# Optimization experiments

Measured on AMD Instinct MI355X. Metric: run time of the kernel, lower is better.

Reference implementation:

```python
import jax, jax.numpy as jnp
import numpy as np

B, C, W, T = 4, 64, 128, 20


def _sinusoid_table(t, c):
    # angle[ch, tau] = tau / 10000^(2*(ch//2)/C); even ch -> sin, odd ch -> cos
    pos = jnp.arange(t, dtype=jnp.float32)                       # [t]
    ch = jnp.arange(c)                                           # [C]
    inv_freq = jnp.power(10000.0, -2.0 * (ch // 2).astype(jnp.float32) / c)  # [C]
    angle = inv_freq[:, None] * pos[None, :]                     # [C, t]
    pe = jnp.where((ch % 2 == 0)[:, None], jnp.sin(angle), jnp.cos(angle))   # [C, t]
    return pe


def setup_inputs() -> dict:
    key = jax.random.key(0)
    x = jax.random.normal(key, (B, C, W, W, T), dtype=jnp.float32)
    return {"x": x, "t": T}


def reference(x, t):
    # x: [B, C, W, W, t]; pos_table broadcast over batch and spatial dims
    pe = _sinusoid_table(t, x.shape[1])          # [C, t]
    return x + pe[None, :, None, None, :]
```

## Files before the change

### kernel.cpp

```cpp
#include <hip/hip_runtime.h>
#include <hip/hip_bf16.h>


#define C_DIM 64
#define T_DIM 20
#define CSTRIDE (128 * 128 * 20)
#define NELEM (4 * 64 * 128 * 128 * 20)
#define NV4 (NELEM / 4)

__global__ __launch_bounds__(256) void pe_add_kernel(const float* __restrict__ x,
                                                     float* __restrict__ out) {
    __shared__ float pe[C_DIM * T_DIM];
    for (int idx = threadIdx.x; idx < C_DIM * T_DIM; idx += blockDim.x) {
        int c = idx / T_DIM;
        int t = idx - c * T_DIM;
        float invf = __powf(10000.0f, -2.0f * (float)(c >> 1) * (1.0f / 64.0f));
        float ang = invf * (float)t;
        pe[idx] = (c & 1) ? cosf(ang) : sinf(ang);
    }
    __syncthreads();

    const float4* __restrict__ x4 = (const float4*)x;
    float4* __restrict__ o4 = (float4*)out;

    unsigned stride = gridDim.x * blockDim.x;
    for (unsigned v = blockIdx.x * blockDim.x + threadIdx.x; v < (unsigned)NV4; v += stride) {
        unsigned i = v * 4u;
        unsigned t0 = i % (unsigned)T_DIM;
        unsigned c = (i / (unsigned)CSTRIDE) & (C_DIM - 1);
        float4 p = *(const float4*)&pe[c * T_DIM + t0];
        float4 xv = x4[v];
        float4 r;
        r.x = xv.x + p.x;
        r.y = xv.y + p.y;
        r.z = xv.z + p.z;
        r.w = xv.w + p.w;
        o4[v] = r;
    }
}

extern "C" void kernel_launch(void* const* d_in, const int* in_sizes, int n_in,
                              void* d_out, int out_size, void* d_ws, size_t ws_size,
                              hipStream_t stream) {
    const float* x = (const float*)d_in[0];
    float* out = (float*)d_out;

    const int block = 256;
    int grid = 2048;
    pe_add_kernel<<<grid, block, 0, stream>>>(x, out);
}
```

Baseline: 545.4 us.

## Compute PE per thread, process all batches per thread, use nontemporal stores

Replaces the grid-stride loop and the shared-memory PE table with one thread per float4 of a batch slice. Each thread computes its four sinusoid values in registers and applies them to the four batch elements, issuing four independent loads. Outputs are written with nontemporal stores to reduce cache pollution. This removes the per-block table setup, the barrier and the div/mod work per element, in exchange for computing trig values directly in every thread.

```diff
diff --git a/kernel.cpp b/kernel.cpp
--- a/kernel.cpp
+++ b/kernel.cpp
@@ -4,39 +4,53 @@
 
 #define C_DIM 64
 #define T_DIM 20
-#define CSTRIDE (128 * 128 * 20)
-#define NELEM (4 * 64 * 128 * 128 * 20)
-#define NV4 (NELEM / 4)
+#define W_DIM 128
+#define CSTRIDE (W_DIM * W_DIM * T_DIM)
+#define BSTRIDE (C_DIM * CSTRIDE)
+#define PER_B_V4 (BSTRIDE / 4)
+#define BLOCKS (PER_B_V4 / 256)
+
+typedef float f32x4 __attribute__((ext_vector_type(4)));
 
 __global__ __launch_bounds__(256) void pe_add_kernel(const float* __restrict__ x,
                                                      float* __restrict__ out) {
-    __shared__ float pe[C_DIM * T_DIM];
-    for (int idx = threadIdx.x; idx < C_DIM * T_DIM; idx += blockDim.x) {
-        int c = idx / T_DIM;
-        int t = idx - c * T_DIM;
-        float invf = __powf(10000.0f, -2.0f * (float)(c >> 1) * (1.0f / 64.0f));
-        float ang = invf * (float)t;
-        pe[idx] = (c & 1) ? cosf(ang) : sinf(ang);
+    unsigned j = blockIdx.x * 256u + threadIdx.x;
+    unsigned i0 = j * 4u;
+    unsigned c = i0 / (unsigned)CSTRIDE;
+    unsigned t0 = i0 % (unsigned)T_DIM;
+
+    float invf = __powf(10000.0f, -2.0f * (float)(c >> 1) * (1.0f / 64.0f));
+    float a0 = invf * (float)t0;
+    f32x4 p;
+    if (c & 1) {
+        p.x = cosf(a0);
+        p.y = cosf(a0 + invf);
+        p.z = cosf(a0 + 2.0f * invf);
+        p.w = cosf(a0 + 3.0f * invf);
+    } else {
+        p.x = sinf(a0);
+        p.y = sinf(a0 + invf);
+        p.z = sinf(a0 + 2.0f * invf);
+        p.w = sinf(a0 + 3.0f * invf);
     }
-    __syncthreads();
 
-    const float4* __restrict__ x4 = (const float4*)x;
-    float4* __restrict__ o4 = (float4*)out;
+    const f32x4* __restrict__ x4 = (const f32x4*)x;
+    f32x4* __restrict__ o4 = (f32x4*)out;
 
-    unsigned stride = gridDim.x * blockDim.x;
-    for (unsigned v = blockIdx.x * blockDim.x + threadIdx.x; v < (unsigned)NV4; v += stride) {
-        unsigned i = v * 4u;
-        unsigned t0 = i % (unsigned)T_DIM;
-        unsigned c = (i / (unsigned)CSTRIDE) & (C_DIM - 1);
-        float4 p = *(const float4*)&pe[c * T_DIM + t0];
-        float4 xv = x4[v];
-        float4 r;
-        r.x = xv.x + p.x;
-        r.y = xv.y + p.y;
-        r.z = xv.z + p.z;
-        r.w = xv.w + p.w;
-        o4[v] = r;
-    }
+    f32x4 v0 = x4[j + 0u * PER_B_V4];
+    f32x4 v1 = x4[j + 1u * PER_B_V4];
+    f32x4 v2 = x4[j + 2u * PER_B_V4];
+    f32x4 v3 = x4[j + 3u * PER_B_V4];
+
+    v0 += p;
+    v1 += p;
+    v2 += p;
+    v3 += p;
+
+    __builtin_nontemporal_store(v0, &o4[j + 0u * PER_B_V4]);
+    __builtin_nontemporal_store(v1, &o4[j + 1u * PER_B_V4]);
+    __builtin_nontemporal_store(v2, &o4[j + 2u * PER_B_V4]);
+    __builtin_nontemporal_store(v3, &o4[j + 3u * PER_B_V4]);
 }
 
 extern "C" void kernel_launch(void* const* d_in, const int* in_sizes, int n_in,
@@ -44,8 +58,5 @@
                               hipStream_t stream) {
     const float* x = (const float*)d_in[0];
     float* out = (float*)d_out;
-
-    const int block = 256;
-    int grid = 2048;
-    pe_add_kernel<<<grid, block, 0, stream>>>(x, out);
+    pe_add_kernel<<<BLOCKS, 256, 0, stream>>>(x, out);
 }
```

Measured after the change: 563.0 us. 1.03x slower.
